# Kernel tuning notes

Hardware: AMD Instinct MI355X
Metric: run time of the kernel (lower is better)

Reference implementation:

```python
import jax, jax.numpy as jnp
import numpy as np

B = 32
HID = 768
OUT5 = 2304          # feature_layers * hidden_size
HDIM = 512
NUM_CLUSTERS = 65536
MAX_GROUP = 11
NUM_LABELS = 670091  # padding index = NUM_LABELS
TOPK = 10


def setup_inputs() -> dict:
    key = jax.random.key(0)
    ks = jax.random.split(key, 10)
    embed = jax.random.normal(ks[8], (NUM_LABELS + 1, HDIM), dtype=jnp.float32) * 0.02
    embed = embed.at[-1].set(0.0)  # padding row is zeros, as in nn.Embedding padding_idx
    return {
        "hid_first": jax.random.normal(ks[0], (B, HID), dtype=jnp.float32),
        "hid_last5": jax.random.normal(ks[1], (B, OUT5), dtype=jnp.float32),
        "W_meta1": jax.random.normal(ks[2], (HID, HDIM), dtype=jnp.float32) * 0.02,
        "b_meta1": jnp.zeros((HDIM,), dtype=jnp.float32),
        "W_meta2": jax.random.normal(ks[3], (HDIM, NUM_CLUSTERS), dtype=jnp.float32) * 0.02,
        "b_meta2": jnp.zeros((NUM_CLUSTERS,), dtype=jnp.float32),
        "W_ext": jax.random.normal(ks[4], (OUT5, HDIM), dtype=jnp.float32) * 0.02,
        "b_ext": jnp.zeros((HDIM,), dtype=jnp.float32),
        "embed": embed,
        "group_y": jax.random.randint(ks[9], (NUM_CLUSTERS, MAX_GROUP), 0, NUM_LABELS + 1, dtype=jnp.int64),
    }


def reference(hid_first, hid_last5, W_meta1, b_meta1, W_meta2, b_meta2,
              W_ext, b_ext, embed, group_y):
    # meta_classifier (eval mode: dropout = identity), exact GELU like torch nn.GELU
    h = jax.nn.gelu(hid_first @ W_meta1 + b_meta1, approximate=False)   # [B, HDIM]
    meta_logits = h @ W_meta2 + b_meta2                                  # [B, NUM_CLUSTERS]

    # get_candidates: sigmoid + topk over meta logits (detached in torch)
    group_scores = jax.nn.sigmoid(jax.lax.stop_gradient(meta_logits))
    scores, indices = jax.lax.top_k(group_scores, TOPK)                  # [B, TOPK]

    cands = group_y[indices]                                             # [B, TOPK, MAX_GROUP]
    cand_scores = jnp.broadcast_to(scores[..., None], cands.shape)
    cands = cands.reshape(cands.shape[0], -1)                            # [B, TOPK*MAX_GROUP]
    cand_scores = cand_scores.reshape(cands.shape)
    valid = cands != NUM_LABELS                                          # padding positions

    # ext_hidden projection of concatenated last-5 CLS features
    h_ext = jax.nn.gelu(hid_last5 @ W_ext + b_ext, approximate=False)    # [B, HDIM]

    # gather candidate label embeddings and batched matvec (torch.bmm)
    W_c = embed[cands]                                                   # [B, C, HDIM]
    logits = jnp.einsum('bch,bh->bc', W_c, h_ext)                        # [B, C]

    # torch maps exactly-zero logits (padding rows) to -inf before sigmoid
    cscores = jax.nn.sigmoid(jnp.where(logits == 0.0, -jnp.inf, logits))
    comb = cscores * jnp.where(valid, cand_scores, 0.0)
    return cands, cscores, comb
```

## Files before the change

### kernel.cpp

```cpp
#include <hip/hip_runtime.h>
#include <hip/hip_bf16.h>
#include <math.h>

#define B_     32
#define HID_   768
#define OUT5_  2304
#define HDIM_  512
#define NC_    65536
#define MAXG_  11
#define NL_    670091
#define TOPK_  10
#define CAND_  110
#define NOUT_  3520

__device__ __forceinline__ float gelu_exact(float x){
  return 0.5f * x * (1.0f + erff(x * 0.70710678118654752440f));
}

__device__ __forceinline__ unsigned long long packv(float x, int col){
  unsigned u = __float_as_uint(x);
  u = (u & 0x80000000u) ? ~u : (u | 0x80000000u);
  return (((unsigned long long)u) << 16) | (unsigned long long)(65535 - col);
}

__device__ __forceinline__ float unpack_val(unsigned long long g){
  unsigned u = (unsigned)(g >> 16);
  unsigned bits = (u & 0x80000000u) ? (u & 0x7FFFFFFFu) : ~u;
  return __uint_as_float(bits);
}

__device__ __forceinline__ int unpack_col(unsigned long long g){
  return 65535 - (int)(g & 0xFFFFULL);
}

__device__ __forceinline__ unsigned long long block_max_u64(unsigned long long m,
                                                            unsigned long long* sm, int nwaves){
  #pragma unroll
  for (int off = 1; off < 64; off <<= 1){
    unsigned long long o = __shfl_xor(m, off);
    if (o > m) m = o;
  }
  const int tid = threadIdx.x;
  if ((tid & 63) == 0) sm[tid >> 6] = m;
  __syncthreads();
  unsigned long long g = sm[0];
  for (int w = 1; w < nwaves; ++w) if (sm[w] > g) g = sm[w];
  __syncthreads();
  return g;
}

typedef const __attribute__((address_space(1))) void* gas_t;
typedef __attribute__((address_space(3))) void* las_t;
__device__ __forceinline__ void gload_lds16(const float* g, float* l){
  __builtin_amdgcn_global_load_lds((gas_t)(const void*)g, (las_t)(void*)l, 16, 0, 0);
}

__global__ __launch_bounds__(256)
void mlp_partial(const float* __restrict__ hidf, const float* __restrict__ hidl5,
                 const float* __restrict__ W1, const float* __restrict__ Wext,
                 float* __restrict__ partial){
  const int jl  = threadIdx.x & 63;
  const int bq  = threadIdx.x >> 6;
  const int col = blockIdx.x * 64 + jl;
  const int chunk = blockIdx.y;
  const float* W; const float* X; int Kfull, k0;
  if (chunk < 8){ W = W1;   X = hidf;  Kfull = HID_;  k0 = chunk * 96; }
  else          { W = Wext; X = hidl5; Kfull = OUT5_; k0 = (chunk - 8) * 96; }
  const float* Wp = W + (size_t)k0 * HDIM_ + col;
  const float* Xp = X + (size_t)(bq * 8) * Kfull + k0;
  float acc[8] = {0,0,0,0,0,0,0,0};
  for (int k = 0; k < 96; k += 8){
    float wv[8];
    #pragma unroll
    for (int u = 0; u < 8; ++u) wv[u] = Wp[(size_t)(k + u) * HDIM_];
    #pragma unroll
    for (int i = 0; i < 8; ++i){
      const float4 xa = *reinterpret_cast<const float4*>(Xp + (size_t)i * Kfull + k);
      const float4 xb = *reinterpret_cast<const float4*>(Xp + (size_t)i * Kfull + k + 4);
      acc[i] = fmaf(xa.x, wv[0], acc[i]);
      acc[i] = fmaf(xa.y, wv[1], acc[i]);
      acc[i] = fmaf(xa.z, wv[2], acc[i]);
      acc[i] = fmaf(xa.w, wv[3], acc[i]);
      acc[i] = fmaf(xb.x, wv[4], acc[i]);
      acc[i] = fmaf(xb.y, wv[5], acc[i]);
      acc[i] = fmaf(xb.z, wv[6], acc[i]);
      acc[i] = fmaf(xb.w, wv[7], acc[i]);
    }
  }
  float* outp = partial + (size_t)chunk * (B_ * HDIM_) + (size_t)(bq * 8) * HDIM_ + col;
  #pragma unroll
  for (int i = 0; i < 8; ++i) outp[(size_t)i * HDIM_] = acc[i];
}

__global__ __launch_bounds__(256)
void act_kernel(const float* __restrict__ partial, const float* __restrict__ b1,
                const float* __restrict__ bext, float* __restrict__ hT,
                float* __restrict__ h_ext){
  const int t = blockIdx.x * 256 + threadIdx.x;
  if (t < B_ * HDIM_){
    const int b = t >> 9, j = t & 511;
    float s = b1[j];
    #pragma unroll
    for (int c = 0; c < 8; ++c) s += partial[c * (B_ * HDIM_) + t];
    hT[j * B_ + b] = gelu_exact(s);
  } else {
    const int u = t - B_ * HDIM_;
    const int j = u & 511;
    float s = bext[j];
    #pragma unroll
    for (int c = 8; c < 32; ++c) s += partial[c * (B_ * HDIM_) + u];
    h_ext[u] = gelu_exact(s);
  }
}

#define CKM_ 32
__global__ __launch_bounds__(1024, 4)
void meta_gemm(const float* __restrict__ hT, const float* __restrict__ W2,
               const float* __restrict__ b2, float* __restrict__ logits){
  __shared__ float smem[3][CKM_ * 256];
  const int tid = threadIdx.x;
  const int l   = tid & 63;
  const int w   = tid >> 6;
  const int r   = w & 3;
  const int q   = w >> 2;
  const int colBase = blockIdx.x * 256;
  const int sb8 = __builtin_amdgcn_readfirstlane(r * 8);
  const int kb8 = __builtin_amdgcn_readfirstlane(q * 8);

  float acc[8][4];
  #pragma unroll
  for (int i = 0; i < 8; ++i)
    #pragma unroll
    for (int j = 0; j < 4; ++j) acc[i][j] = 0.f;

  auto stage = [&](int c, int bf){
    #pragma unroll
    for (int i = 0; i < 2; ++i){
      const int row = 2 * w + i;
      gload_lds16(W2 + (size_t)(c * CKM_ + row) * NC_ + colBase + l * 4,
                  &smem[bf][row * 256]);
    }
  };

  auto compute = [&](int c, int bf){
    const float* __restrict__ hbase = hT + (size_t)(c * CKM_ + kb8) * B_ + sb8;
    #pragma unroll
    for (int kk = 0; kk < 8; ++kk){
      const float4 wv = *reinterpret_cast<const float4*>(&smem[bf][(kb8 + kk) * 256 + l * 4]);
      const float4 h0 = *reinterpret_cast<const float4*>(hbase + kk * B_);
      const float4 h1 = *reinterpret_cast<const float4*>(hbase + kk * B_ + 4);
      const float hv[8] = {h0.x, h0.y, h0.z, h0.w, h1.x, h1.y, h1.z, h1.w};
      #pragma unroll
      for (int row = 0; row < 8; ++row){
        acc[row][0] = fmaf(hv[row], wv.x, acc[row][0]);
        acc[row][1] = fmaf(hv[row], wv.y, acc[row][1]);
        acc[row][2] = fmaf(hv[row], wv.z, acc[row][2]);
        acc[row][3] = fmaf(hv[row], wv.w, acc[row][3]);
      }
    }
  };

  stage(0, 0);
  stage(1, 1);
  for (int c = 0; c < HDIM_ / CKM_ - 1; ++c){
    asm volatile("s_waitcnt vmcnt(2)" ::: "memory");
    __builtin_amdgcn_s_barrier();
    if (c + 2 < HDIM_ / CKM_) stage(c + 2, (c + 2) % 3);
    compute(c, c % 3);
  }
  asm volatile("s_waitcnt vmcnt(0)" ::: "memory");
  __builtin_amdgcn_s_barrier();
  compute(HDIM_ / CKM_ - 1, (HDIM_ / CKM_ - 1) % 3);
  __syncthreads();

  #pragma unroll
  for (int qq = 1; qq <= 3; ++qq){
    if (q == qq){
      #pragma unroll
      for (int row = 0; row < 8; ++row){
        float4 t; t.x = acc[row][0]; t.y = acc[row][1]; t.z = acc[row][2]; t.w = acc[row][3];
        *reinterpret_cast<float4*>(&smem[0][(r * 8 + row) * 256 + l * 4]) = t;
      }
    }
    __syncthreads();
    if (q == 0){
      #pragma unroll
      for (int row = 0; row < 8; ++row){
        const float4 t = *reinterpret_cast<const float4*>(&smem[0][(r * 8 + row) * 256 + l * 4]);
        acc[row][0] += t.x; acc[row][1] += t.y; acc[row][2] += t.z; acc[row][3] += t.w;
      }
    }
    __syncthreads();
  }

  if (q == 0){
    const float4 bb = *reinterpret_cast<const float4*>(b2 + colBase + l * 4);
    #pragma unroll
    for (int row = 0; row < 8; ++row){
      float4 o;
      o.x = acc[row][0] + bb.x; o.y = acc[row][1] + bb.y;
      o.z = acc[row][2] + bb.z; o.w = acc[row][3] + bb.w;
      *reinterpret_cast<float4*>(logits + (size_t)(sb8 + row) * NC_ + colBase + l * 4) = o;
    }
  }
}

__global__ __launch_bounds__(256)
void topk_seg(const float* __restrict__ logits, float* __restrict__ segv,
              int* __restrict__ segi){
  __shared__ unsigned long long sm[4];
  const int b   = blockIdx.x >> 3;
  const int seg = blockIdx.x & 7;
  const int tid = threadIdx.x;
  const float* row = logits + (size_t)b * NC_ + seg * 8192;
  float v[10]; int ix[10];
  #pragma unroll
  for (int r = 0; r < 10; ++r){ v[r] = -INFINITY; ix[r] = -1; }
  for (int s = 0; s < 32; ++s){
    const int j = s * 256 + tid;
    const float x = row[j];
    if (x > v[9]){
      v[9] = x; ix[9] = seg * 8192 + j;
      #pragma unroll
      for (int p = 9; p > 0; --p){
        if (v[p] > v[p-1]){
          float tv = v[p]; v[p] = v[p-1]; v[p-1] = tv;
          int   ti = ix[p]; ix[p] = ix[p-1]; ix[p-1] = ti;
        }
      }
    }
  }
  for (int r = 0; r < 10; ++r){
    unsigned long long mp = (ix[0] >= 0) ? packv(v[0], ix[0]) : 0ULL;
    unsigned long long g  = block_max_u64(mp, sm, 4);
    if (mp == g && mp != 0ULL){
      #pragma unroll
      for (int q = 0; q < 9; ++q){ v[q] = v[q+1]; ix[q] = ix[q+1]; }
      v[9] = -INFINITY; ix[9] = -1;
    }
    if (tid == 0){
      segv[blockIdx.x * 10 + r] = unpack_val(g);
      segi[blockIdx.x * 10 + r] = unpack_col(g);
    }
  }
}

__global__ __launch_bounds__(128)
void topk_merge(const float* __restrict__ segv, const int* __restrict__ segi,
                int* __restrict__ tk_idx, float* __restrict__ tk_score){
  __shared__ unsigned long long sm[2];
  const int b   = blockIdx.x;
  const int tid = threadIdx.x;
  unsigned long long mp = 0ULL;
  if (tid < 80) mp = packv(segv[b * 80 + tid], segi[b * 80 + tid]);
  for (int r = 0; r < 10; ++r){
    unsigned long long g = block_max_u64(mp, sm, 2);
    if (mp == g && mp != 0ULL) mp = 0ULL;
    if (tid == 0){
      tk_idx[b * TOPK_ + r]   = unpack_col(g);
      tk_score[b * TOPK_ + r] = 1.0f / (1.0f + expf(-unpack_val(g)));
    }
  }
}

__global__ __launch_bounds__(256)
void cand_kernel(const int* __restrict__ gy, const float* __restrict__ embed,
                 const float* __restrict__ h_ext, const int* __restrict__ tk_idx,
                 const float* __restrict__ tk_score, float* __restrict__ out_f){
  const int wid  = threadIdx.x >> 6;
  const int lane = threadIdx.x & 63;
  const int gw   = blockIdx.x * 4 + wid;
  const int b    = gw / CAND_;
  const int c    = gw - b * CAND_;
  const int t    = c / MAXG_;
  const int g    = c - t * MAXG_;

  const unsigned int* gyw = (const unsigned int*)gy;
  const unsigned int probe = gyw[2 * (size_t)(gw * 64 + lane) + 1];
  const bool is64 = (__ballot(probe != 0u) == 0ULL);

  const int idx  = tk_idx[b * TOPK_ + t];
  const size_t li = (size_t)idx * MAXG_ + g;
  const int cand = is64 ? (int)((const long long*)gy)[li] : gy[li];

  const float* erow = embed + (size_t)cand * HDIM_;
  const float* hrow = h_ext + (size_t)b * HDIM_;
  const float4 e0 = reinterpret_cast<const float4*>(erow)[lane];
  const float4 e1 = reinterpret_cast<const float4*>(erow)[lane + 64];
  const float4 h0 = reinterpret_cast<const float4*>(hrow)[lane];
  const float4 h1 = reinterpret_cast<const float4*>(hrow)[lane + 64];
  float s = e0.x*h0.x + e0.y*h0.y + e0.z*h0.z + e0.w*h0.w
          + e1.x*h1.x + e1.y*h1.y + e1.z*h1.z + e1.w*h1.w;
  #pragma unroll
  for (int off = 1; off < 64; off <<= 1) s += __shfl_xor(s, off);
  if (lane == 0){
    const float cs   = (s == 0.0f) ? 0.0f : 1.0f / (1.0f + expf(-s));
    const float comb = cs * ((cand != NL_) ? tk_score[b * TOPK_ + t] : 0.0f);
    const int o = b * CAND_ + c;
    __hip_bfloat16* outs = (__hip_bfloat16*)(out_f + NOUT_);
    __hip_bfloat16* outm = outs + NOUT_;
    out_f[o] = (float)cand;
    outs[o]  = __float2bfloat16(cs);
    outm[o]  = __float2bfloat16(comb);
  }
}

extern "C" void kernel_launch(void* const* d_in, const int* in_sizes, int n_in,
                              void* d_out, int out_size, void* d_ws, size_t ws_size,
                              hipStream_t stream){
  const float* hidf  = (const float*)d_in[0];
  const float* hidl5 = (const float*)d_in[1];
  const float* W1    = (const float*)d_in[2];
  const float* b1    = (const float*)d_in[3];
  const float* W2    = (const float*)d_in[4];
  const float* b2    = (const float*)d_in[5];
  const float* Wext  = (const float*)d_in[6];
  const float* bext  = (const float*)d_in[7];
  const float* embed = (const float*)d_in[8];
  const int*   gy    = (const int*)d_in[9];
  float* out_f = (float*)d_out;

  float* ws      = (float*)d_ws;
  float* logits  = ws;
  float* partial = ws;
  float* hT      = logits + (size_t)B_ * NC_;
  float* h_ext   = hT + B_ * HDIM_;
  float* segv    = h_ext + B_ * HDIM_;
  int*   segi    = (int*)(segv + 2560);
  float* tk_sc   = (float*)(segi + 2560);
  int*   tk_ix   = (int*)(tk_sc + 320);

  mlp_partial<<<dim3(8, 32), 256, 0, stream>>>(hidf, hidl5, W1, Wext, partial);
  act_kernel <<<128, 256, 0, stream>>>(partial, b1, bext, hT, h_ext);
  meta_gemm  <<<NC_ / 256, 1024, 0, stream>>>(hT, W2, b2, logits);
  topk_seg   <<<B_ * 8, 256, 0, stream>>>(logits, segv, segi);
  topk_merge <<<B_, 128, 0, stream>>>(segv, segi, tk_ix, tk_sc);
  cand_kernel<<<NOUT_ / 4, 256, 0, stream>>>(gy, embed, h_ext, tk_ix, tk_sc, out_f);
}
```

Measured before the change: 81.57 us.

## Fuse top-k merge and candidate scoring into one per-batch kernel

Combines the final top-k merge and the candidate embedding dot-product kernels into a single kernel with one 1024-thread block per batch row. Top-k indices and scores stay in shared memory instead of round-tripping through global memory, and one kernel launch is removed. In exchange, candidate gathers are spread over only 32 blocks, with each wave looping over several candidates, which reduces memory-level parallelism for the random embedding row loads.

```diff
diff --git a/kernel.cpp b/kernel.cpp
--- a/kernel.cpp
+++ b/kernel.cpp
@@ -245,63 +245,71 @@
   }
 }
 
-__global__ __launch_bounds__(128)
-void topk_merge(const float* __restrict__ segv, const int* __restrict__ segi,
-                int* __restrict__ tk_idx, float* __restrict__ tk_score){
-  __shared__ unsigned long long sm[2];
-  const int b   = blockIdx.x;
-  const int tid = threadIdx.x;
+__global__ __launch_bounds__(1024)
+void merge_cand(const float* __restrict__ segv, const int* __restrict__ segi,
+                const int* __restrict__ gy, const float* __restrict__ embed,
+                const float* __restrict__ h_ext, float* __restrict__ out_f){
+  __shared__ unsigned long long smx[16];
+  __shared__ int   tk_i[TOPK_];
+  __shared__ float tk_s[TOPK_];
+  const int b    = blockIdx.x;
+  const int tid  = threadIdx.x;
+  const int lane = tid & 63;
+  const int w    = tid >> 6;
+
   unsigned long long mp = 0ULL;
   if (tid < 80) mp = packv(segv[b * 80 + tid], segi[b * 80 + tid]);
   for (int r = 0; r < 10; ++r){
-    unsigned long long g = block_max_u64(mp, sm, 2);
-    if (mp == g && mp != 0ULL) mp = 0ULL;
+    unsigned long long wm = mp;
+    #pragma unroll
+    for (int off = 1; off < 64; off <<= 1){
+      unsigned long long o = __shfl_xor(wm, off);
+      if (o > wm) wm = o;
+    }
+    if (lane == 0) smx[w] = wm;
+    __syncthreads();
+    unsigned long long g = smx[0];
+    #pragma unroll
+    for (int qq = 1; qq < 16; ++qq) if (smx[qq] > g) g = smx[qq];
+    if (mp == g && g != 0ULL) mp = 0ULL;
     if (tid == 0){
-      tk_idx[b * TOPK_ + r]   = unpack_col(g);
-      tk_score[b * TOPK_ + r] = 1.0f / (1.0f + expf(-unpack_val(g)));
-    }
-  }
-}
-
-__global__ __launch_bounds__(256)
-void cand_kernel(const int* __restrict__ gy, const float* __restrict__ embed,
-                 const float* __restrict__ h_ext, const int* __restrict__ tk_idx,
-                 const float* __restrict__ tk_score, float* __restrict__ out_f){
-  const int wid  = threadIdx.x >> 6;
-  const int lane = threadIdx.x & 63;
-  const int gw   = blockIdx.x * 4 + wid;
-  const int b    = gw / CAND_;
-  const int c    = gw - b * CAND_;
-  const int t    = c / MAXG_;
-  const int g    = c - t * MAXG_;
+      tk_i[r] = unpack_col(g);
+      tk_s[r] = 1.0f / (1.0f + expf(-unpack_val(g)));
+    }
+    __syncthreads();
+  }
 
   const unsigned int* gyw = (const unsigned int*)gy;
-  const unsigned int probe = gyw[2 * (size_t)(gw * 64 + lane) + 1];
+  const unsigned int probe = gyw[2 * (size_t)((b * 16 + w) * 64 + lane) + 1];
   const bool is64 = (__ballot(probe != 0u) == 0ULL);
 
-  const int idx  = tk_idx[b * TOPK_ + t];
-  const size_t li = (size_t)idx * MAXG_ + g;
-  const int cand = is64 ? (int)((const long long*)gy)[li] : gy[li];
-
-  const float* erow = embed + (size_t)cand * HDIM_;
   const float* hrow = h_ext + (size_t)b * HDIM_;
-  const float4 e0 = reinterpret_cast<const float4*>(erow)[lane];
-  const float4 e1 = reinterpret_cast<const float4*>(erow)[lane + 64];
   const float4 h0 = reinterpret_cast<const float4*>(hrow)[lane];
   const float4 h1 = reinterpret_cast<const float4*>(hrow)[lane + 64];
-  float s = e0.x*h0.x + e0.y*h0.y + e0.z*h0.z + e0.w*h0.w
-          + e1.x*h1.x + e1.y*h1.y + e1.z*h1.z + e1.w*h1.w;
-  #pragma unroll
-  for (int off = 1; off < 64; off <<= 1) s += __shfl_xor(s, off);
-  if (lane == 0){
-    const float cs   = (s == 0.0f) ? 0.0f : 1.0f / (1.0f + expf(-s));
-    const float comb = cs * ((cand != NL_) ? tk_score[b * TOPK_ + t] : 0.0f);
-    const int o = b * CAND_ + c;
-    __hip_bfloat16* outs = (__hip_bfloat16*)(out_f + NOUT_);
-    __hip_bfloat16* outm = outs + NOUT_;
-    out_f[o] = (float)cand;
-    outs[o]  = __float2bfloat16(cs);
-    outm[o]  = __float2bfloat16(comb);
+  __hip_bfloat16* outs = (__hip_bfloat16*)(out_f + NOUT_);
+  __hip_bfloat16* outm = outs + NOUT_;
+
+  for (int c = w; c < CAND_; c += 16){
+    const int t = c / MAXG_;
+    const int g = c - t * MAXG_;
+    const int idx = tk_i[t];
+    const size_t li = (size_t)idx * MAXG_ + g;
+    const int cand = is64 ? (int)((const long long*)gy)[li] : gy[li];
+    const float* erow = embed + (size_t)cand * HDIM_;
+    const float4 e0 = reinterpret_cast<const float4*>(erow)[lane];
+    const float4 e1 = reinterpret_cast<const float4*>(erow)[lane + 64];
+    float s = e0.x*h0.x + e0.y*h0.y + e0.z*h0.z + e0.w*h0.w
+            + e1.x*h1.x + e1.y*h1.y + e1.z*h1.z + e1.w*h1.w;
+    #pragma unroll
+    for (int off = 1; off < 64; off <<= 1) s += __shfl_xor(s, off);
+    if (lane == 0){
+      const float cs   = (s == 0.0f) ? 0.0f : 1.0f / (1.0f + expf(-s));
+      const float comb = cs * ((cand != NL_) ? tk_s[t] : 0.0f);
+      const int o = b * CAND_ + c;
+      out_f[o] = (float)cand;
+      outs[o]  = __float2bfloat16(cs);
+      outm[o]  = __float2bfloat16(comb);
+    }
   }
 }
 
@@ -327,13 +335,10 @@
   float* h_ext   = hT + B_ * HDIM_;
   float* segv    = h_ext + B_ * HDIM_;
   int*   segi    = (int*)(segv + 2560);
-  float* tk_sc   = (float*)(segi + 2560);
-  int*   tk_ix   = (int*)(tk_sc + 320);
 
   mlp_partial<<<dim3(8, 32), 256, 0, stream>>>(hidf, hidl5, W1, Wext, partial);
   act_kernel <<<128, 256, 0, stream>>>(partial, b1, bext, hT, h_ext);
   meta_gemm  <<<NC_ / 256, 1024, 0, stream>>>(hT, W2, b2, logits);
   topk_seg   <<<B_ * 8, 256, 0, stream>>>(logits, segv, segi);
-  topk_merge <<<B_, 128, 0, stream>>>(segv, segi, tk_ix, tk_sc);
-  cand_kernel<<<NOUT_ / 4, 256, 0, stream>>>(gy, embed, h_ext, tk_ix, tk_sc, out_f);
-}
+  merge_cand <<<B_, 1024, 0, stream>>>(segv, segi, gy, embed, h_ext, out_f);
+}
```

Result: slower. 100.3 us (+23.0%).

## Fuse per-stripe max into meta GEMM epilogue and prune top-k to winning stripes

Applied to the files above, without the earlier changes.

The meta GEMM epilogue now computes a packed max per 256-column stripe for each batch row and stores it. A single top-k kernel per row then picks the 10 stripes with the largest maxima and scans only those 2560 columns instead of all 65536. This is exact, because each of the true top-10 values lies in a stripe whose max is among the 10 largest stripe maxima. It removes the full-row scan and the separate merge kernel, which cuts logits reads and one launch, at the cost of extra shuffle reductions in the GEMM epilogue.

```diff
diff --git a/kernel.cpp b/kernel.cpp
--- a/kernel.cpp
+++ b/kernel.cpp
@@ -12,6 +12,7 @@
 #define TOPK_  10
 #define CAND_  110
 #define NOUT_  3520
+#define NSTR_  256
 
 __device__ __forceinline__ float gelu_exact(float x){
   return 0.5f * x * (1.0f + erff(x * 0.70710678118654752440f));
@@ -33,13 +34,18 @@
   return 65535 - (int)(g & 0xFFFFULL);
 }
 
-__device__ __forceinline__ unsigned long long block_max_u64(unsigned long long m,
-                                                            unsigned long long* sm, int nwaves){
+__device__ __forceinline__ unsigned long long wave_max_u64(unsigned long long m){
   #pragma unroll
   for (int off = 1; off < 64; off <<= 1){
     unsigned long long o = __shfl_xor(m, off);
     if (o > m) m = o;
   }
+  return m;
+}
+
+__device__ __forceinline__ unsigned long long block_max_u64(unsigned long long m,
+                                                            unsigned long long* sm, int nwaves){
+  m = wave_max_u64(m);
   const int tid = threadIdx.x;
   if ((tid & 63) == 0) sm[tid >> 6] = m;
   __syncthreads();
@@ -116,7 +122,8 @@
 #define CKM_ 32
 __global__ __launch_bounds__(1024, 4)
 void meta_gemm(const float* __restrict__ hT, const float* __restrict__ W2,
-               const float* __restrict__ b2, float* __restrict__ logits){
+               const float* __restrict__ b2, float* __restrict__ logits,
+               unsigned long long* __restrict__ blockmax){
   __shared__ float smem[3][CKM_ * 256];
   const int tid = threadIdx.x;
   const int l   = tid & 63;
@@ -201,26 +208,45 @@
       o.x = acc[row][0] + bb.x; o.y = acc[row][1] + bb.y;
       o.z = acc[row][2] + bb.z; o.w = acc[row][3] + bb.w;
       *reinterpret_cast<float4*>(logits + (size_t)(sb8 + row) * NC_ + colBase + l * 4) = o;
+      unsigned long long k0 = packv(o.x, colBase + l * 4);
+      unsigned long long k1 = packv(o.y, colBase + l * 4 + 1);
+      unsigned long long k2 = packv(o.z, colBase + l * 4 + 2);
+      unsigned long long k3 = packv(o.w, colBase + l * 4 + 3);
+      unsigned long long m01 = k0 > k1 ? k0 : k1;
+      unsigned long long m23 = k2 > k3 ? k2 : k3;
+      unsigned long long m = wave_max_u64(m01 > m23 ? m01 : m23);
+      if (l == 0) blockmax[(size_t)(sb8 + row) * NSTR_ + blockIdx.x] = m;
     }
   }
 }
 
 __global__ __launch_bounds__(256)
-void topk_seg(const float* __restrict__ logits, float* __restrict__ segv,
-              int* __restrict__ segi){
+void stripe_topk(const float* __restrict__ logits,
+                 const unsigned long long* __restrict__ blockmax,
+                 int* __restrict__ tk_idx, float* __restrict__ tk_score){
   __shared__ unsigned long long sm[4];
-  const int b   = blockIdx.x >> 3;
-  const int seg = blockIdx.x & 7;
+  __shared__ int win[TOPK_];
+  const int b   = blockIdx.x;
   const int tid = threadIdx.x;
-  const float* row = logits + (size_t)b * NC_ + seg * 8192;
+
+  unsigned long long mp = blockmax[(size_t)b * NSTR_ + tid];
+  for (int r = 0; r < 10; ++r){
+    unsigned long long g = block_max_u64(mp, sm, 4);
+    if (mp == g && g != 0ULL) mp = 0ULL;
+    if (tid == 0) win[r] = unpack_col(g) >> 8;
+    __syncthreads();
+  }
+
+  const float* row = logits + (size_t)b * NC_;
   float v[10]; int ix[10];
   #pragma unroll
   for (int r = 0; r < 10; ++r){ v[r] = -INFINITY; ix[r] = -1; }
-  for (int s = 0; s < 32; ++s){
-    const int j = s * 256 + tid;
-    const float x = row[j];
+  #pragma unroll
+  for (int i = 0; i < 10; ++i){
+    const int col = win[i] * 256 + tid;
+    const float x = row[col];
     if (x > v[9]){
-      v[9] = x; ix[9] = seg * 8192 + j;
+      v[9] = x; ix[9] = col;
       #pragma unroll
       for (int p = 9; p > 0; --p){
         if (v[p] > v[p-1]){
@@ -231,31 +257,13 @@
     }
   }
   for (int r = 0; r < 10; ++r){
-    unsigned long long mp = (ix[0] >= 0) ? packv(v[0], ix[0]) : 0ULL;
-    unsigned long long g  = block_max_u64(mp, sm, 4);
-    if (mp == g && mp != 0ULL){
-      #pragma unroll
-      for (int q = 0; q < 9; ++q){ v[q] = v[q+1]; ix[q] = ix[q+1]; }
+    unsigned long long mp2 = (ix[0] >= 0) ? packv(v[0], ix[0]) : 0ULL;
+    unsigned long long g = block_max_u64(mp2, sm, 4);
+    if (mp2 == g && mp2 != 0ULL){
+      #pragma unroll
+      for (int p = 0; p < 9; ++p){ v[p] = v[p+1]; ix[p] = ix[p+1]; }
       v[9] = -INFINITY; ix[9] = -1;
     }
-    if (tid == 0){
-      segv[blockIdx.x * 10 + r] = unpack_val(g);
-      segi[blockIdx.x * 10 + r] = unpack_col(g);
-    }
-  }
-}
-
-__global__ __launch_bounds__(128)
-void topk_merge(const float* __restrict__ segv, const int* __restrict__ segi,
-                int* __restrict__ tk_idx, float* __restrict__ tk_score){
-  __shared__ unsigned long long sm[2];
-  const int b   = blockIdx.x;
-  const int tid = threadIdx.x;
-  unsigned long long mp = 0ULL;
-  if (tid < 80) mp = packv(segv[b * 80 + tid], segi[b * 80 + tid]);
-  for (int r = 0; r < 10; ++r){
-    unsigned long long g = block_max_u64(mp, sm, 2);
-    if (mp == g && mp != 0ULL) mp = 0ULL;
     if (tid == 0){
       tk_idx[b * TOPK_ + r]   = unpack_col(g);
       tk_score[b * TOPK_ + r] = 1.0f / (1.0f + expf(-unpack_val(g)));
@@ -325,15 +333,14 @@
   float* partial = ws;
   float* hT      = logits + (size_t)B_ * NC_;
   float* h_ext   = hT + B_ * HDIM_;
-  float* segv    = h_ext + B_ * HDIM_;
-  int*   segi    = (int*)(segv + 2560);
-  float* tk_sc   = (float*)(segi + 2560);
+  unsigned long long* blockmax =
+      (unsigned long long*)(h_ext + B_ * HDIM_);
+  float* tk_sc   = (float*)(blockmax + (size_t)B_ * NSTR_);
   int*   tk_ix   = (int*)(tk_sc + 320);
 
   mlp_partial<<<dim3(8, 32), 256, 0, stream>>>(hidf, hidl5, W1, Wext, partial);
   act_kernel <<<128, 256, 0, stream>>>(partial, b1, bext, hT, h_ext);
-  meta_gemm  <<<NC_ / 256, 1024, 0, stream>>>(hT, W2, b2, logits);
-  topk_seg   <<<B_ * 8, 256, 0, stream>>>(logits, segv, segi);
-  topk_merge <<<B_, 128, 0, stream>>>(segv, segi, tk_ix, tk_sc);
+  meta_gemm  <<<NC_ / 256, 1024, 0, stream>>>(hT, W2, b2, logits, blockmax);
+  stripe_topk<<<B_, 256, 0, stream>>>(logits, blockmax, tk_ix, tk_sc);
   cand_kernel<<<NOUT_ / 4, 256, 0, stream>>>(gy, embed, h_ext, tk_ix, tk_sc, out_f);
 }
```

Result: faster. 74.53 us, median of 2 (-8.6%).
